# Kernel optimization log

Hardware: AMD Instinct MI355X
Metric: run time of the kernel (lower is better)

The kernel has to match this reference:

```python
import jax, jax.numpy as jnp
import numpy as np
import math

MAX_SIZE = 2048  # max_size init arg


def setup_inputs() -> dict:
    key = jax.random.key(0)
    k1, k2, k3 = jax.random.split(key, 3)
    B, S, D = 16, 1024, 512
    PRED = 256
    data = jax.random.normal(k1, (B, S, D), dtype=jnp.float32)
    W = jax.random.normal(k2, (PRED, D), dtype=jnp.float32) * (1.0 / math.sqrt(D))
    b = jax.random.normal(k3, (PRED,), dtype=jnp.float32) * 0.01
    return {"data": data, "W": W, "b": b}


def reference(data, W, b):
    # data: [B, S, D]; self-attention with q=k=v=data
    B, S, D = data.shape
    pred_len = W.shape[0]
    scale = 1.0 / math.sqrt(D)
    scores = jnp.einsum('bsd,btd->bst', data, data) * scale          # [B,S,S]
    prob = jax.nn.softmax(scores, axis=-1)
    attn = jnp.einsum('bst,btd->bsd', prob, data)                     # [B,S,D]
    # NOTE: the original concatenates a 'mask' block (rows S..2S) onto attn,
    # but the per-timestep Linear loop only reads rows 0..S-1, so the mask
    # never affects the output (dead code). The loop collapses to one GEMM.
    lin = jnp.einsum('bsd,pd->bsp', attn, W) + b                      # [B,S,pred_len]
    out = jnp.zeros((B, MAX_SIZE, pred_len), dtype=data.dtype)
    out = out.at[:, :S, :].set(lin)
    return out
```

## Files before the change

kernel.cpp:

```cpp
#include <hip/hip_runtime.h>
#include <cstdint>
#include <cstddef>

#define B_    16
#define S_    1024
#define D_    512
#define P_    256
#define MAXS_ 2048

typedef unsigned short u16;
typedef unsigned int   u32;
typedef _Float16 f16;
typedef _Float16 f16x8 __attribute__((ext_vector_type(8)));
typedef float  f32x4  __attribute__((ext_vector_type(4)));
typedef unsigned short u16x4 __attribute__((ext_vector_type(4)));
typedef unsigned short u16x8 __attribute__((ext_vector_type(8)));

__device__ __forceinline__ void gld_lds16(const void* g, void* l) {
  __builtin_amdgcn_global_load_lds(
      (const __attribute__((address_space(1))) u32*)g,
      (__attribute__((address_space(3))) u32*)l, 16, 0, 0);
}

__device__ __forceinline__ u16 f2h(float f) {
  return __builtin_bit_cast(u16, (f16)f);
}
__device__ __forceinline__ float h2f(u16 h) {
  return (float)__builtin_bit_cast(f16, h);
}

__global__ void convert_f16_kernel(const float* __restrict__ src, u16* __restrict__ dst, long n4) {
  long stride = (long)gridDim.x * blockDim.x;
  for (long i = (long)blockIdx.x * blockDim.x + threadIdx.x; i < n4; i += stride) {
    float4 v = ((const float4*)src)[i];
    u16x4 o;
    o[0] = f2h(v.x); o[1] = f2h(v.y); o[2] = f2h(v.z); o[3] = f2h(v.w);
    ((u16x4*)dst)[i] = o;
  }
}

__global__ __launch_bounds__(512, 2) void qk_pipe(
    const u16* __restrict__ A, u16* __restrict__ Cout, float scale) {
  extern __shared__ __align__(16) char smem[];
  const int tid  = threadIdx.x;
  const int lane = tid & 63;
  const int w    = tid >> 6;
  const int wm   = w >> 2;
  const int wn   = w & 3;
  const int lr   = lane & 15;
  const int hi   = lane >> 4;

  const int bz = blockIdx.z;
  const int I0 = blockIdx.y * 256;
  const int J0 = blockIdx.x * 256;
  const u16* Ab = A + (long)bz * (S_ * D_);

  auto stageP = [&](int s, int part) {
    if (s >= 16) return;
    char* dst = smem + (s & 3) * 32768 + part * 16384;
    const int base = part ? J0 : I0;
    const int k0 = s * 32;
    #pragma unroll
    for (int i = 0; i < 2; ++i) {
      int cid   = i * 512 + tid;
      int inner = cid >> 2;
      int c     = (cid & 3) ^ ((inner >> 1) & 3);
      gld_lds16(Ab + (size_t)(base + inner) * D_ + k0 + c * 8, dst + cid * 16);
    }
  };

  f32x4 acc[8][4] = {};

  stageP(0, 0); stageP(0, 1);
  stageP(1, 0); stageP(1, 1);
  stageP(2, 0); stageP(2, 1);
  asm volatile("s_waitcnt vmcnt(8)" ::: "memory");
  __builtin_amdgcn_s_barrier();

  for (int s = 0; s < 16; ++s) {
    const char* sl = smem + (s & 3) * 32768;
    f16x8 bf[4];
    {
      f16x8 af[4];
      #pragma unroll
      for (int mq = 0; mq < 4; ++mq) {
        int row = wm * 128 + mq * 16 + lr;
        int cp  = hi ^ ((row >> 1) & 3);
        af[mq] = *(const f16x8*)(sl + row * 64 + cp * 16);
      }
      #pragma unroll
      for (int n = 0; n < 4; ++n) {
        int row = wn * 64 + n * 16 + lr;
        int cp  = hi ^ ((row >> 1) & 3);
        bf[n] = *(const f16x8*)(sl + 16384 + row * 64 + cp * 16);
      }
      stageP(s + 3, 0);
      __builtin_amdgcn_s_barrier();
      asm volatile("s_waitcnt lgkmcnt(0)" ::: "memory");
      __builtin_amdgcn_sched_barrier(0);
      __builtin_amdgcn_s_setprio(1);
      #pragma unroll
      for (int mq = 0; mq < 4; ++mq)
        #pragma unroll
        for (int n = 0; n < 4; ++n)
          acc[mq][n] = __builtin_amdgcn_mfma_f32_16x16x32_f16(af[mq], bf[n], acc[mq][n], 0, 0, 0);
      __builtin_amdgcn_s_setprio(0);
      __builtin_amdgcn_s_barrier();
    }
    {
      f16x8 af[4];
      #pragma unroll
      for (int mq = 0; mq < 4; ++mq) {
        int row = wm * 128 + 64 + mq * 16 + lr;
        int cp  = hi ^ ((row >> 1) & 3);
        af[mq] = *(const f16x8*)(sl + row * 64 + cp * 16);
      }
      stageP(s + 3, 1);
      __builtin_amdgcn_s_barrier();
      asm volatile("s_waitcnt lgkmcnt(0)" ::: "memory");
      __builtin_amdgcn_sched_barrier(0);
      __builtin_amdgcn_s_setprio(1);
      #pragma unroll
      for (int mq = 0; mq < 4; ++mq)
        #pragma unroll
        for (int n = 0; n < 4; ++n)
          acc[4 + mq][n] = __builtin_amdgcn_mfma_f32_16x16x32_f16(af[mq], bf[n], acc[4 + mq][n], 0, 0, 0);
      __builtin_amdgcn_s_setprio(0);
      if (s <= 12)      asm volatile("s_waitcnt vmcnt(8)" ::: "memory");
      else if (s == 13) asm volatile("s_waitcnt vmcnt(4)" ::: "memory");
      else if (s == 14) asm volatile("s_waitcnt vmcnt(0)" ::: "memory");
      __builtin_amdgcn_s_barrier();
    }
  }

  u16* Cb = Cout + (long)bz * S_ * S_;
  const int row0 = I0 + wm * 128;
  const int col0 = J0 + wn * 64;
  #pragma unroll
  for (int m = 0; m < 8; ++m) {
    #pragma unroll
    for (int i = 0; i < 4; ++i) {
      int r = row0 + m * 16 + (hi << 2) + i;
      #pragma unroll
      for (int n = 0; n < 4; ++n) {
        int c = col0 + n * 16 + lr;
        Cb[(size_t)r * S_ + c] = f2h(acc[m][n][i] * scale);
      }
    }
  }
}

__global__ __launch_bounds__(256) void stats_kernel(
    const u16* __restrict__ scores, float2* __restrict__ rowstat) {
  const int lane = threadIdx.x & 63;
  const int wv   = threadIdx.x >> 6;
  const long row = (long)blockIdx.x * 4 + wv;
  const u16* src = scores + row * S_;

  u16x8 a0 = *(const u16x8*)&src[lane * 16];
  u16x8 a1 = *(const u16x8*)&src[lane * 16 + 8];
  float v[16];
  #pragma unroll
  for (int j = 0; j < 8; ++j) { v[j] = h2f(a0[j]); v[8 + j] = h2f(a1[j]); }

  float mx = v[0];
  #pragma unroll
  for (int j = 1; j < 16; ++j) mx = fmaxf(mx, v[j]);
  #pragma unroll
  for (int off = 32; off > 0; off >>= 1)
    mx = fmaxf(mx, __shfl_xor(mx, off));

  const float l2e = 1.4426950408889634f;
  float sum = 0.f;
  #pragma unroll
  for (int j = 0; j < 16; ++j) sum += exp2f((v[j] - mx) * l2e);
  #pragma unroll
  for (int off = 32; off > 0; off >>= 1)
    sum += __shfl_xor(sum, off);

  if (lane == 0) rowstat[row] = make_float2(mx, 1.f / sum);
}

__global__ __launch_bounds__(256, 2) void pv_kernel(
    const u16* __restrict__ scores, const u16* __restrict__ VWT,
    const float2* __restrict__ rowstat,
    float* __restrict__ out, const float* __restrict__ bias) {
  extern __shared__ __align__(16) char smem[];
  const int tid  = threadIdx.x;
  const int lane = tid & 63;
  const int wn   = tid >> 6;
  const int bz = blockIdx.z;
  const int yt = blockIdx.y;

  float* ob = out + (long)bz * MAXS_ * P_;
  if (yt >= 16) {
    float4* o = (float4*)(ob + (size_t)yt * 64 * P_);
    for (int i = tid; i < 64 * P_ / 4; i += 256)
      o[i] = make_float4(0.f, 0.f, 0.f, 0.f);
    return;
  }

  const int q0 = yt * 64;
  const u16* sb = scores + ((long)bz * S_ + q0) * S_;
  const u16* Vb = VWT + (long)bz * P_ * S_;

  const int arow = tid >> 2;
  const int ac   = tid & 3;
  float2 st = rowstat[(long)bz * S_ + q0 + arow];
  const float am = st.x, ail = st.y;
  const float l2e = 1.4426950408889634f;

  auto stageB = [&](int t) {
    char* dB = smem + 16384 + (t & 1) * 32768;
    const int k0 = t * 64;
    #pragma unroll
    for (int i = 0; i < 8; ++i) {
      int cid = i * 256 + tid;
      int row = cid >> 3;
      int c   = (cid & 7) ^ (row & 7);
      gld_lds16(Vb + (size_t)row * S_ + k0 + c * 8, dB + cid * 16);
    }
  };
  auto writeA = [&](int buf, u16x8 r0, u16x8 r1) {
    u16x8 p0, p1;
    #pragma unroll
    for (int j = 0; j < 8; ++j) {
      p0[j] = f2h(exp2f((h2f(r0[j]) - am) * l2e) * ail);
      p1[j] = f2h(exp2f((h2f(r1[j]) - am) * l2e) * ail);
    }
    int c0 = (ac * 2)     ^ (arow & 7);
    int c1 = (ac * 2 + 1) ^ (arow & 7);
    *(u16x8*)(smem + buf * 8192 + (arow * 8 + c0) * 16) = p0;
    *(u16x8*)(smem + buf * 8192 + (arow * 8 + c1) * 16) = p1;
  };

  f32x4 acc[4][4] = {};
  u16x8 a0, a1;

  a0 = *(const u16x8*)(sb + (size_t)arow * S_ + ac * 16);
  a1 = *(const u16x8*)(sb + (size_t)arow * S_ + ac * 16 + 8);
  __builtin_amdgcn_sched_barrier(0);
  stageB(0);
  __builtin_amdgcn_sched_barrier(0);
  asm volatile("s_waitcnt vmcnt(0)" ::: "memory");
  writeA(0, a0, a1);
  asm volatile("s_waitcnt lgkmcnt(0)" ::: "memory");
  __builtin_amdgcn_s_barrier();

  for (int t = 0; t < 16; ++t) {
    const char* lA = smem + (t & 1) * 8192;
    const char* lB = smem + 16384 + (t & 1) * 32768;

    if (t < 15) {
      a0 = *(const u16x8*)(sb + (size_t)arow * S_ + (t + 1) * 64 + ac * 16);
      a1 = *(const u16x8*)(sb + (size_t)arow * S_ + (t + 1) * 64 + ac * 16 + 8);
      __builtin_amdgcn_sched_barrier(0);
      stageB(t + 1);
      __builtin_amdgcn_sched_barrier(0);
    }

    #pragma unroll
    for (int kk = 0; kk < 2; ++kk) {
      f16x8 af[4], bf[4];
      #pragma unroll
      for (int m = 0; m < 4; ++m) {
        int row = m * 16 + (lane & 15);
        int cp  = (kk * 4 + (lane >> 4)) ^ (row & 7);
        af[m] = *(const f16x8*)(lA + ((row * 8 + cp) << 4));
      }
      #pragma unroll
      for (int n = 0; n < 4; ++n) {
        int row = wn * 64 + n * 16 + (lane & 15);
        int cp  = (kk * 4 + (lane >> 4)) ^ (row & 7);
        bf[n] = *(const f16x8*)(lB + ((row * 8 + cp) << 4));
      }
      __builtin_amdgcn_s_setprio(1);
      #pragma unroll
      for (int m = 0; m < 4; ++m)
        #pragma unroll
        for (int n = 0; n < 4; ++n)
          acc[m][n] = __builtin_amdgcn_mfma_f32_16x16x32_f16(af[m], bf[n], acc[m][n], 0, 0, 0);
      __builtin_amdgcn_s_setprio(0);
    }

    if (t < 15) {
      asm volatile("s_waitcnt vmcnt(0)" ::: "memory");
      writeA((t + 1) & 1, a0, a1);
      asm volatile("s_waitcnt lgkmcnt(0)" ::: "memory");
      __builtin_amdgcn_s_barrier();
    }
  }

  const int lr = lane & 15, hi = lane >> 4;
  const int col0 = wn * 64;
  float bv[4];
  #pragma unroll
  for (int n = 0; n < 4; ++n) bv[n] = bias[col0 + n * 16 + lr];
  #pragma unroll
  for (int m = 0; m < 4; ++m) {
    #pragma unroll
    for (int i = 0; i < 4; ++i) {
      int r = q0 + m * 16 + (hi << 2) + i;
      #pragma unroll
      for (int n = 0; n < 4; ++n)
        ob[(size_t)r * P_ + col0 + n * 16 + lr] = acc[m][n][i] + bv[n];
    }
  }
}

template<int KK, int BM, int BN, int NW, int WNS>
__global__ __launch_bounds__(NW * 64, 1) void gemm_nt_small(
    const u16* __restrict__ A, const u16* __restrict__ Bm,
    u16* __restrict__ C, long sAb, long sBb, long sCb, int LDC) {
  constexpr int T   = NW * 64;
  constexpr int WMS = NW / WNS;
  constexpr int MF  = BM / (WMS * 16);
  constexpr int NF  = BN / (WNS * 16);
  constexpr int LA  = BM * 8 / T;
  constexpr int LB  = BN * 8 / T;
  constexpr int SZ  = (BM + BN) * 128;
  constexpr int NT  = KK / 64;

  extern __shared__ __align__(16) char smem[];
  const int tid  = threadIdx.x;
  const int lane = tid & 63;
  const int w    = tid >> 6;
  const int wm   = w / WNS;
  const int wn   = w % WNS;
  const int lr   = lane & 15;
  const int hi   = lane >> 4;

  const int bz = blockIdx.z;
  const int I0 = blockIdx.y * BM;
  const int J0 = blockIdx.x * BN;
  const u16* Ab = A  + (long)bz * sAb;
  const u16* Bb = Bm + (long)bz * sBb;

  auto stage = [&](int buf, int k0) {
    char* sA = smem + buf * SZ;
    char* sB = sA + BM * 128;
    #pragma unroll
    for (int i = 0; i < LA; ++i) {
      int cid = i * T + tid;
      int row = cid >> 3;
      int c   = (cid & 7) ^ (row & 7);
      gld_lds16(Ab + (size_t)(I0 + row) * KK + k0 + c * 8, sA + cid * 16);
    }
    #pragma unroll
    for (int i = 0; i < LB; ++i) {
      int cid = i * T + tid;
      int row = cid >> 3;
      int c   = (cid & 7) ^ (row & 7);
      gld_lds16(Bb + (size_t)(J0 + row) * KK + k0 + c * 8, sB + cid * 16);
    }
  };

  f32x4 acc[MF][NF] = {};
  stage(0, 0);
  for (int t = 0; t < NT; ++t) {
    const char* lA = smem + (t & 1) * SZ;
    const char* lB = lA + BM * 128;
    if (t + 1 < NT) {
      stage((t + 1) & 1, (t + 1) * 64);
      asm volatile("s_waitcnt vmcnt(%0)" :: "i"(LA + LB) : "memory");
    } else {
      asm volatile("s_waitcnt vmcnt(0)" ::: "memory");
    }
    __builtin_amdgcn_s_barrier();
    __builtin_amdgcn_sched_barrier(0);
    #pragma unroll
    for (int kk = 0; kk < 2; ++kk) {
      f16x8 af[MF], bfv[NF];
      #pragma unroll
      for (int m = 0; m < MF; ++m) {
        int row = wm * (MF * 16) + m * 16 + lr;
        int cp  = (kk * 4 + hi) ^ (row & 7);
        af[m] = *(const f16x8*)(lA + ((row * 8 + cp) << 4));
      }
      #pragma unroll
      for (int n = 0; n < NF; ++n) {
        int row = wn * (NF * 16) + n * 16 + lr;
        int cp  = (kk * 4 + hi) ^ (row & 7);
        bfv[n] = *(const f16x8*)(lB + ((row * 8 + cp) << 4));
      }
      __builtin_amdgcn_s_setprio(1);
      #pragma unroll
      for (int m = 0; m < MF; ++m)
        #pragma unroll
        for (int n = 0; n < NF; ++n)
          acc[m][n] = __builtin_amdgcn_mfma_f32_16x16x32_f16(af[m], bfv[n], acc[m][n], 0, 0, 0);
      __builtin_amdgcn_s_setprio(0);
    }
    __builtin_amdgcn_sched_barrier(0);
    __builtin_amdgcn_s_barrier();
  }

  const int row0 = I0 + wm * (MF * 16);
  const int col0 = J0 + wn * (NF * 16);
  #pragma unroll
  for (int m = 0; m < MF; ++m)
    #pragma unroll
    for (int i = 0; i < 4; ++i) {
      int r = row0 + m * 16 + (hi << 2) + i;
      #pragma unroll
      for (int n = 0; n < NF; ++n)
        C[(long)bz * sCb + (size_t)r * LDC + col0 + n * 16 + lr] = f2h(acc[m][n][i]);
    }
}

extern "C" void kernel_launch(void* const* d_in, const int* in_sizes, int n_in,
                              void* d_out, int out_size, void* d_ws, size_t ws_size,
                              hipStream_t stream) {
  const float* data = (const float*)d_in[0];
  const float* W    = (const float*)d_in[1];
  const float* bias = (const float*)d_in[2];
  float* out = (float*)d_out;
  char*  ws  = (char*)d_ws;

  const size_t MB = 1024 * 1024;
  u16*    dataH   = (u16*)(ws);
  u16*    Wh      = (u16*)(ws + 16 * MB);
  u16*    scoresH = (u16*)(ws + 17 * MB);
  u16*    VWT     = (u16*)(ws + 49 * MB);
  float2* rowstat = (float2*)(ws + 57 * MB);

  const float scale = 0.04419417382415922f;

  constexpr int SMEM_QK = 4 * 32768;
  constexpr int SMEM_PV = 2 * 8192 + 2 * 32768;
  constexpr int SMEM_VW = 2 * (64 + 256) * 128;

  (void)hipFuncSetAttribute((const void*)&qk_pipe,
                      hipFuncAttributeMaxDynamicSharedMemorySize, SMEM_QK);
  (void)hipFuncSetAttribute((const void*)&pv_kernel,
                      hipFuncAttributeMaxDynamicSharedMemorySize, SMEM_PV);
  (void)hipFuncSetAttribute((const void*)&gemm_nt_small<512, 64, 256, 2, 2>,
                      hipFuncAttributeMaxDynamicSharedMemorySize, SMEM_VW);

  convert_f16_kernel<<<2048, 256, 0, stream>>>(data, dataH, (long)B_ * S_ * D_ / 4);
  convert_f16_kernel<<<64, 256, 0, stream>>>(W, Wh, (long)P_ * D_ / 4);

  gemm_nt_small<512, 64, 256, 2, 2><<<dim3(4, 4, 16), 128, SMEM_VW, stream>>>(
      Wh, dataH, VWT, 0L, (long)S_ * D_, (long)P_ * S_, S_);

  qk_pipe<<<dim3(4, 4, 16), 512, SMEM_QK, stream>>>(dataH, scoresH, scale);

  stats_kernel<<<4096, 256, 0, stream>>>(scoresH, rowstat);

  pv_kernel<<<dim3(1, 32, 16), 256, SMEM_PV, stream>>>(
      scoresH, VWT, rowstat, out, bias);
}
```

Before: 91.37 us.

## Rewrite PV kernel as 4-stage ring pipeline and retile VW GEMM

```diff
diff --git a/kernel.cpp b/kernel.cpp
--- a/kernel.cpp
+++ b/kernel.cpp
@@ -27,6 +27,13 @@
 }
 __device__ __forceinline__ float h2f(u16 h) {
   return (float)__builtin_bit_cast(f16, h);
+}
+
+template<int N> __device__ __forceinline__ void waitvm() {
+  if constexpr (N == 0)      asm volatile("s_waitcnt vmcnt(0)" ::: "memory");
+  else if constexpr (N == 4) asm volatile("s_waitcnt vmcnt(4)" ::: "memory");
+  else if constexpr (N == 5) asm volatile("s_waitcnt vmcnt(5)" ::: "memory");
+  else static_assert(N == 0, "unsupported vmcnt literal");
 }
 
 __global__ void convert_f16_kernel(const float* __restrict__ src, u16* __restrict__ dst, long n4) {
@@ -181,16 +188,18 @@
   if (lane == 0) rowstat[row] = make_float2(mx, 1.f / sum);
 }
 
-__global__ __launch_bounds__(256, 2) void pv_kernel(
+__global__ __launch_bounds__(256, 1) void pv_ring(
     const u16* __restrict__ scores, const u16* __restrict__ VWT,
     const float2* __restrict__ rowstat,
     float* __restrict__ out, const float* __restrict__ bias) {
   extern __shared__ __align__(16) char smem[];
   const int tid  = threadIdx.x;
   const int lane = tid & 63;
-  const int wn   = tid >> 6;
-  const int bz = blockIdx.z;
-  const int yt = blockIdx.y;
+  const int wv   = tid >> 6;
+  const int lr   = lane & 15;
+  const int hi   = lane >> 4;
+  const int bz   = blockIdx.z;
+  const int yt   = blockIdx.y;
 
   float* ob = out + (long)bz * MAXS_ * P_;
   if (yt >= 16) {
@@ -203,96 +212,114 @@
   const int q0 = yt * 64;
   const u16* sb = scores + ((long)bz * S_ + q0) * S_;
   const u16* Vb = VWT + (long)bz * P_ * S_;
-
   const int arow = tid >> 2;
   const int ac   = tid & 3;
-  float2 st = rowstat[(long)bz * S_ + q0 + arow];
+  const float2 st = rowstat[(long)bz * S_ + q0 + arow];
   const float am = st.x, ail = st.y;
   const float l2e = 1.4426950408889634f;
 
-  auto stageB = [&](int t) {
-    char* dB = smem + 16384 + (t & 1) * 32768;
-    const int k0 = t * 64;
-    #pragma unroll
-    for (int i = 0; i < 8; ++i) {
+  auto loadA = [&](int s) -> u16x8 {
+    return *(const u16x8*)(sb + (size_t)arow * S_ + s * 32 + ac * 8);
+  };
+  auto writeA = [&](int s, u16x8 r) {
+    u16x8 p;
+    #pragma unroll
+    for (int j = 0; j < 8; ++j)
+      p[j] = f2h(exp2f((h2f(r[j]) - am) * l2e) * ail);
+    *(u16x8*)(smem + (s & 3) * 4096 + arow * 64 + ac * 16) = p;
+  };
+  auto stageB = [&](int s) {
+    char* dB = smem + 16384 + (s & 3) * 16384;
+    const int k0 = s * 32;
+    #pragma unroll
+    for (int i = 0; i < 4; ++i) {
       int cid = i * 256 + tid;
-      int row = cid >> 3;
-      int c   = (cid & 7) ^ (row & 7);
-      gld_lds16(Vb + (size_t)row * S_ + k0 + c * 8, dB + cid * 16);
-    }
-  };
-  auto writeA = [&](int buf, u16x8 r0, u16x8 r1) {
-    u16x8 p0, p1;
-    #pragma unroll
-    for (int j = 0; j < 8; ++j) {
-      p0[j] = f2h(exp2f((h2f(r0[j]) - am) * l2e) * ail);
-      p1[j] = f2h(exp2f((h2f(r1[j]) - am) * l2e) * ail);
-    }
-    int c0 = (ac * 2)     ^ (arow & 7);
-    int c1 = (ac * 2 + 1) ^ (arow & 7);
-    *(u16x8*)(smem + buf * 8192 + (arow * 8 + c0) * 16) = p0;
-    *(u16x8*)(smem + buf * 8192 + (arow * 8 + c1) * 16) = p1;
+      gld_lds16(Vb + (size_t)(cid >> 2) * S_ + k0 + (cid & 3) * 8, dB + cid * 16);
+    }
+  };
+  auto fragRead = [&](int s, f16x8 (&af)[4], f16x8 (&bf)[4]) {
+    const char* aB = smem + (s & 3) * 4096;
+    const char* bB = smem + 16384 + (s & 3) * 16384;
+    #pragma unroll
+    for (int m = 0; m < 4; ++m)
+      af[m] = *(const f16x8*)(aB + (m * 16 + lr) * 64 + hi * 16);
+    #pragma unroll
+    for (int n = 0; n < 4; ++n)
+      bf[n] = *(const f16x8*)(bB + (wv * 64 + n * 16 + lr) * 64 + hi * 16);
   };
 
   f32x4 acc[4][4] = {};
-  u16x8 a0, a1;
-
-  a0 = *(const u16x8*)(sb + (size_t)arow * S_ + ac * 16);
-  a1 = *(const u16x8*)(sb + (size_t)arow * S_ + ac * 16 + 8);
-  __builtin_amdgcn_sched_barrier(0);
-  stageB(0);
-  __builtin_amdgcn_sched_barrier(0);
-  asm volatile("s_waitcnt vmcnt(0)" ::: "memory");
-  writeA(0, a0, a1);
+  auto mfma16 = [&](f16x8 (&af)[4], f16x8 (&bf)[4]) {
+    __builtin_amdgcn_s_setprio(1);
+    #pragma unroll
+    for (int m = 0; m < 4; ++m)
+      #pragma unroll
+      for (int n = 0; n < 4; ++n)
+        acc[m][n] = __builtin_amdgcn_mfma_f32_16x16x32_f16(af[m], bf[n], acc[m][n], 0, 0, 0);
+    __builtin_amdgcn_s_setprio(0);
+  };
+
+  f16x8 aF0[4], bF0[4], aF1[4], bF1[4];
+  u16x8 rA0, rA1, rA2, rA3;
+
+  rA0 = loadA(0); rA1 = loadA(1); rA2 = loadA(2); rA3 = loadA(3);
+  __builtin_amdgcn_sched_barrier(0);
+  stageB(0); stageB(1); stageB(2);
+  __builtin_amdgcn_sched_barrier(0);
+  waitvm<4>();
+  writeA(0, rA0); writeA(1, rA1);
   asm volatile("s_waitcnt lgkmcnt(0)" ::: "memory");
   __builtin_amdgcn_s_barrier();
-
-  for (int t = 0; t < 16; ++t) {
-    const char* lA = smem + (t & 1) * 8192;
-    const char* lB = smem + 16384 + (t & 1) * 32768;
-
-    if (t < 15) {
-      a0 = *(const u16x8*)(sb + (size_t)arow * S_ + (t + 1) * 64 + ac * 16);
-      a1 = *(const u16x8*)(sb + (size_t)arow * S_ + (t + 1) * 64 + ac * 16 + 8);
-      __builtin_amdgcn_sched_barrier(0);
-      stageB(t + 1);
-      __builtin_amdgcn_sched_barrier(0);
-    }
-
-    #pragma unroll
-    for (int kk = 0; kk < 2; ++kk) {
-      f16x8 af[4], bf[4];
-      #pragma unroll
-      for (int m = 0; m < 4; ++m) {
-        int row = m * 16 + (lane & 15);
-        int cp  = (kk * 4 + (lane >> 4)) ^ (row & 7);
-        af[m] = *(const f16x8*)(lA + ((row * 8 + cp) << 4));
-      }
-      #pragma unroll
-      for (int n = 0; n < 4; ++n) {
-        int row = wn * 64 + n * 16 + (lane & 15);
-        int cp  = (kk * 4 + (lane >> 4)) ^ (row & 7);
-        bf[n] = *(const f16x8*)(lB + ((row * 8 + cp) << 4));
-      }
-      __builtin_amdgcn_s_setprio(1);
-      #pragma unroll
-      for (int m = 0; m < 4; ++m)
-        #pragma unroll
-        for (int n = 0; n < 4; ++n)
-          acc[m][n] = __builtin_amdgcn_mfma_f32_16x16x32_f16(af[m], bf[n], acc[m][n], 0, 0, 0);
-      __builtin_amdgcn_s_setprio(0);
-    }
-
-    if (t < 15) {
-      asm volatile("s_waitcnt vmcnt(0)" ::: "memory");
-      writeA((t + 1) & 1, a0, a1);
-      asm volatile("s_waitcnt lgkmcnt(0)" ::: "memory");
-      __builtin_amdgcn_s_barrier();
-    }
-  }
-
-  const int lr = lane & 15, hi = lane >> 4;
-  const int col0 = wn * 64;
+  fragRead(0, aF0, bF0);
+  asm volatile("s_waitcnt lgkmcnt(0)" ::: "memory");
+  __builtin_amdgcn_sched_barrier(0);
+
+  auto slot = [&](int s, u16x8& dstA, u16x8 srcA,
+                  f16x8 (&afc)[4], f16x8 (&bfc)[4],
+                  f16x8 (&afn)[4], f16x8 (&bfn)[4]) {
+    dstA = loadA(s + 4);
+    __builtin_amdgcn_sched_barrier(0);
+    stageB(s + 3);
+    __builtin_amdgcn_sched_barrier(0);
+    fragRead(s + 1, afn, bfn);
+    mfma16(afc, bfc);
+    waitvm<5>();
+    writeA(s + 2, srcA);
+    asm volatile("s_waitcnt lgkmcnt(0)" ::: "memory");
+    __builtin_amdgcn_s_barrier();
+    __builtin_amdgcn_sched_barrier(0);
+  };
+
+  for (int s0 = 0; s0 < 28; s0 += 4) {
+    slot(s0 + 0, rA0, rA2, aF0, bF0, aF1, bF1);
+    slot(s0 + 1, rA1, rA3, aF1, bF1, aF0, bF0);
+    slot(s0 + 2, rA2, rA0, aF0, bF0, aF1, bF1);
+    slot(s0 + 3, rA3, rA1, aF1, bF1, aF0, bF0);
+  }
+
+  stageB(31);
+  __builtin_amdgcn_sched_barrier(0);
+  fragRead(29, aF1, bF1);
+  mfma16(aF0, bF0);
+  waitvm<4>();
+  writeA(30, rA2);
+  asm volatile("s_waitcnt lgkmcnt(0)" ::: "memory");
+  __builtin_amdgcn_s_barrier();
+  __builtin_amdgcn_sched_barrier(0);
+  fragRead(30, aF0, bF0);
+  mfma16(aF1, bF1);
+  waitvm<0>();
+  writeA(31, rA3);
+  asm volatile("s_waitcnt lgkmcnt(0)" ::: "memory");
+  __builtin_amdgcn_s_barrier();
+  __builtin_amdgcn_sched_barrier(0);
+  fragRead(31, aF1, bF1);
+  mfma16(aF0, bF0);
+  asm volatile("s_waitcnt lgkmcnt(0)" ::: "memory");
+  __builtin_amdgcn_sched_barrier(0);
+  mfma16(aF1, bF1);
+
+  const int col0 = wv * 64;
   float bv[4];
   #pragma unroll
   for (int n = 0; n < 4; ++n) bv[n] = bias[col0 + n * 16 + lr];
@@ -309,7 +336,7 @@
 }
 
 template<int KK, int BM, int BN, int NW, int WNS>
-__global__ __launch_bounds__(NW * 64, 1) void gemm_nt_small(
+__global__ __launch_bounds__(NW * 64, 2) void gemm_nt_small(
     const u16* __restrict__ A, const u16* __restrict__ Bm,
     u16* __restrict__ C, long sAb, long sBb, long sCb, int LDC) {
   constexpr int T   = NW * 64;
@@ -427,26 +454,26 @@
   const float scale = 0.04419417382415922f;
 
   constexpr int SMEM_QK = 4 * 32768;
-  constexpr int SMEM_PV = 2 * 8192 + 2 * 32768;
-  constexpr int SMEM_VW = 2 * (64 + 256) * 128;
+  constexpr int SMEM_PV = 4 * 4096 + 4 * 16384;
+  constexpr int SMEM_VW = 2 * (64 + 128) * 128;
 
   (void)hipFuncSetAttribute((const void*)&qk_pipe,
                       hipFuncAttributeMaxDynamicSharedMemorySize, SMEM_QK);
-  (void)hipFuncSetAttribute((const void*)&pv_kernel,
+  (void)hipFuncSetAttribute((const void*)&pv_ring,
                       hipFuncAttributeMaxDynamicSharedMemorySize, SMEM_PV);
-  (void)hipFuncSetAttribute((const void*)&gemm_nt_small<512, 64, 256, 2, 2>,
+  (void)hipFuncSetAttribute((const void*)&gemm_nt_small<512, 64, 128, 4, 2>,
                       hipFuncAttributeMaxDynamicSharedMemorySize, SMEM_VW);
 
   convert_f16_kernel<<<2048, 256, 0, stream>>>(data, dataH, (long)B_ * S_ * D_ / 4);
   convert_f16_kernel<<<64, 256, 0, stream>>>(W, Wh, (long)P_ * D_ / 4);
 
-  gemm_nt_small<512, 64, 256, 2, 2><<<dim3(4, 4, 16), 128, SMEM_VW, stream>>>(
+  gemm_nt_small<512, 64, 128, 4, 2><<<dim3(8, 4, 16), 256, SMEM_VW, stream>>>(
       Wh, dataH, VWT, 0L, (long)S_ * D_, (long)P_ * S_, S_);
 
   qk_pipe<<<dim3(4, 4, 16), 512, SMEM_QK, stream>>>(dataH, scoresH, scale);
 
   stats_kernel<<<4096, 256, 0, stream>>>(scoresH, rowstat);
 
-  pv_kernel<<<dim3(1, 32, 16), 256, SMEM_PV, stream>>>(
+  pv_ring<<<dim3(1, 32, 16), 256, SMEM_PV, stream>>>(
       scoresH, VWT, rowstat, out, bias);
 }
```

After: 104.6 us. +14.5%, slower.
